# Optimization experiments

Hardware: AMD Instinct MI355X
Metric: run time of the kernel (lower is better)

The kernel has to match this reference:

```python
import jax, jax.numpy as jnp
import numpy as np

H = 4096          # hidden_size
NH = 32           # num_attention_heads
NKV = 2           # multi_query_group_num (kv heads)
HD = 128          # kv_channels / head_dim
RD = 64           # rotary_dim = head_dim * rotary_percent(0.5)
T = 2048          # total tokens (single prefill sequence)
EPS = 1e-5        # layernorm_epsilon
ROPE_BASE = 10000.0


def setup_inputs() -> dict:
    key = jax.random.key(0)
    k0, k1, k2, k3 = jax.random.split(key, 4)
    qkv_out = (NH + 2 * NKV) * HD  # 4608
    return {
        "positions": jnp.arange(T, dtype=jnp.int32),
        "hidden_states": jax.random.normal(k0, (T, H), jnp.float32),
        "w_qkv": jax.random.normal(k1, (qkv_out, H), jnp.float32) * 0.02,
        "b_qkv": jax.random.normal(k2, (qkv_out,), jnp.float32) * 0.02,
        "w_dense": jax.random.normal(k3, (H, NH * HD), jnp.float32) * 0.02,
        "q_ln_w": jnp.ones((HD,), jnp.float32),
        "k_ln_w": jnp.ones((HD,), jnp.float32),
    }


def _rmsnorm(x, w):
    # per-head RMSNorm over head_dim
    return x * jax.lax.rsqrt(jnp.mean(x * x, axis=-1, keepdims=True) + EPS) * w


def _rope(x, positions):
    # partial rotary (first RD dims), interleaved GPT-J style (is_neox_style=False)
    inv_freq = 1.0 / (ROPE_BASE ** (jnp.arange(0, RD, 2, dtype=jnp.float32) / RD))
    ang = positions.astype(jnp.float32)[:, None] * inv_freq      # [T, RD//2]
    cos = jnp.cos(ang)[:, None, :]                               # [T, 1, RD//2]
    sin = jnp.sin(ang)[:, None, :]
    x_rot, x_pass = x[..., :RD], x[..., RD:]
    x1 = x_rot[..., 0::2]
    x2 = x_rot[..., 1::2]
    r1 = x1 * cos - x2 * sin
    r2 = x2 * cos + x1 * sin
    x_rot = jnp.stack([r1, r2], axis=-1).reshape(x.shape[:-1] + (RD,))
    return jnp.concatenate([x_rot, x_pass], axis=-1)


def reference(positions, hidden_states, w_qkv, b_qkv, w_dense, q_ln_w, k_ln_w):
    qkv = hidden_states @ w_qkv.T + b_qkv                        # [T, 4608]
    q_size, kv_size = NH * HD, NKV * HD
    q = qkv[:, :q_size].reshape(T, NH, HD)
    k = qkv[:, q_size:q_size + kv_size].reshape(T, NKV, HD)
    v = qkv[:, q_size + kv_size:].reshape(T, NKV, HD)
    # optional qk layernorm (RMSNorm since config.rmsnorm)
    q = _rmsnorm(q, q_ln_w)
    k = _rmsnorm(k, k_ln_w)
    # rotary embedding
    q = _rope(q, positions)
    k = _rope(k, positions)
    # GQA: expand kv heads to query heads
    group = NH // NKV
    k_exp = jnp.repeat(k, group, axis=1)                         # [T, NH, HD]
    v_exp = jnp.repeat(v, group, axis=1)
    scale = HD ** -0.5
    scores = jnp.einsum("thd,shd->hts", q, k_exp) * scale        # [NH, T, T]
    causal = jnp.tril(jnp.ones((T, T), dtype=bool))
    scores = jnp.where(causal[None, :, :], scores, jnp.finfo(scores.dtype).min)
    attn = jax.nn.softmax(scores, axis=-1)
    out = jnp.einsum("hts,shd->thd", attn, v_exp).reshape(T, NH * HD)
    return out @ w_dense.T                                       # [T, H]
```

## Files before the change

kernel.cpp:

```cpp
#include <hip/hip_runtime.h>
#include <cstdint>
#include <cstddef>

typedef short short4v __attribute__((ext_vector_type(4)));
typedef short short8v __attribute__((ext_vector_type(8)));
typedef float f32x4   __attribute__((ext_vector_type(4)));

#define T_LEN  2048
#define HDIM   4096
#define NHEADS 32
#define HEADD  128
#define QKVN   4608

static __device__ __forceinline__ short f2bf(float f) {
  __bf16 h = (__bf16)f;
  return __builtin_bit_cast(short, h);
}

static __device__ __forceinline__ void gload_lds16(const void* g, void* l) {
  __builtin_amdgcn_global_load_lds((const __attribute__((address_space(1))) void*)g,
                                   (__attribute__((address_space(3))) void*)l,
                                   16, 0, 0);
}

__global__ void cast_f32_to_bf16(const float* __restrict__ in, short* __restrict__ out, int n4) {
  int idx = blockIdx.x * blockDim.x + threadIdx.x;
  int stride = gridDim.x * blockDim.x;
  const float4* in4 = (const float4*)in;
  short4v* out4 = (short4v*)out;
  for (int i = idx; i < n4; i += stride) {
    float4 v = in4[i];
    short4v o;
    o[0] = f2bf(v.x); o[1] = f2bf(v.y); o[2] = f2bf(v.z); o[3] = f2bf(v.w);
    out4[i] = o;
  }
}

__global__ __launch_bounds__(256, 2) void gemm_bt(
    const short* __restrict__ A,
    const short* __restrict__ B,
    const float* __restrict__ bias,
    float* __restrict__ Cout,
    int M, int N, int K)
{
  __shared__ short sA[2][128 * 64];
  __shared__ short sB[2][128 * 64];
  const int tid  = threadIdx.x;
  const int lane = tid & 63;
  const int wv   = tid >> 6;
  const int wr   = wv >> 1;
  const int wc   = wv & 1;
  const int bn0  = blockIdx.x * 128;
  const int bm0  = blockIdx.y * 128;

  const int fr  = lane & 15;
  const int fkb = (lane >> 4) << 4;
  const int swz = (fr & 7) << 4;

  const int c_row  = tid >> 3;
  const int c_colb = (tid & 7) << 4;
  const int c_scol = (c_colb ^ ((c_row & 7) << 4)) >> 1;

  f32x4 zero = {0.f, 0.f, 0.f, 0.f};
  f32x4 acc[4][4];
#pragma unroll
  for (int m = 0; m < 4; m++)
#pragma unroll
    for (int n = 0; n < 4; n++) acc[m][n] = zero;

  auto STAGE = [&](int b, int kt) {
#pragma unroll
    for (int i = 0; i < 4; i++) {
      const int row = i * 32 + c_row;
      gload_lds16(A + (size_t)(bm0 + row) * K + kt + c_scol,
                  (char*)&sA[b][0] + (size_t)(i * 256 + wv * 64) * 16);
    }
#pragma unroll
    for (int i = 0; i < 4; i++) {
      const int row = i * 32 + c_row;
      gload_lds16(B + (size_t)(bn0 + row) * K + kt + c_scol,
                  (char*)&sB[b][0] + (size_t)(i * 256 + wv * 64) * 16);
    }
  };

  int cur = 0;
  STAGE(0, 0);
  __syncthreads();

  for (int kt = 0; kt < K; kt += 64) {
    if (kt + 64 < K) STAGE(cur ^ 1, kt + 64);
    const char* aB = (const char*)&sA[cur][0];
    const char* bB = (const char*)&sB[cur][0];
#pragma unroll
    for (int ks = 0; ks < 2; ks++) {
      short8v af[4], bfr[4];
#pragma unroll
      for (int m = 0; m < 4; m++) {
        const int row = wr * 64 + m * 16 + fr;
        af[m] = *(const short8v*)(aB + row * 128 + ((ks * 64 + fkb) ^ swz));
      }
#pragma unroll
      for (int n = 0; n < 4; n++) {
        const int row = wc * 64 + n * 16 + fr;
        bfr[n] = *(const short8v*)(bB + row * 128 + ((ks * 64 + fkb) ^ swz));
      }
#pragma unroll
      for (int m = 0; m < 4; m++)
#pragma unroll
        for (int n = 0; n < 4; n++)
          acc[m][n] = __builtin_amdgcn_mfma_f32_16x16x32_bf16(af[m], bfr[n], acc[m][n], 0, 0, 0);
    }
    __syncthreads();
    cur ^= 1;
  }

  const int rg = (lane >> 4) * 4;
#pragma unroll
  for (int m = 0; m < 4; m++) {
#pragma unroll
    for (int n = 0; n < 4; n++) {
      const int gcol = bn0 + wc * 64 + n * 16 + fr;
      const float bv = bias ? bias[gcol] : 0.0f;
#pragma unroll
      for (int j = 0; j < 4; j++) {
        const int grow = bm0 + wr * 64 + m * 16 + rg + j;
        Cout[(size_t)grow * N + gcol] = acc[m][n][j] + bv;
      }
    }
  }
}

__global__ __launch_bounds__(64) void qkv_post_kernel(
    const float* __restrict__ qkvf,
    const int*   __restrict__ positions,
    const float* __restrict__ q_ln,
    const float* __restrict__ k_ln,
    short* __restrict__ Qb,
    short* __restrict__ Kb,
    short* __restrict__ Vt)
{
  const int t = blockIdx.x;
  const int h = blockIdx.y;
  const int lane = threadIdx.x;
  const float2 x2 = ((const float2*)(qkvf + (size_t)t * QKVN + h * HEADD))[lane];
  float x = x2.x, y = x2.y;

  if (h >= 34) {
    const int hv = h - 34;
    short* dst = Vt + ((size_t)hv * HEADD + 2 * lane) * T_LEN + t;
    dst[0]     = f2bf(x);
    dst[T_LEN] = f2bf(y);
    return;
  }

  float ss = x * x + y * y;
#pragma unroll
  for (int d = 32; d > 0; d >>= 1) ss += __shfl_xor(ss, d);
  const float r = rsqrtf(ss * (1.0f / 128.0f) + 1e-5f);
  const float* lnw = (h < 32) ? q_ln : k_ln;
  x = x * r * lnw[2 * lane];
  y = y * r * lnw[2 * lane + 1];

  if (lane < 32) {
    const float pos = (float)positions[t];
    const float ang = pos * powf(10000.0f, -(float)lane * (1.0f / 32.0f));
    const float c = cosf(ang), s = sinf(ang);
    const float r1 = x * c - y * s;
    const float r2 = y * c + x * s;
    x = r1; y = r2;
  }

  short* dst = (h < 32) ? (Qb + ((size_t)h * T_LEN + t) * HEADD + 2 * lane)
                        : (Kb + ((size_t)(h - 32) * T_LEN + t) * HEADD + 2 * lane);
  dst[0] = f2bf(x);
  dst[1] = f2bf(y);
}

__global__ __launch_bounds__(256, 2) void attn_kernel(
    const short* __restrict__ Qb,
    const short* __restrict__ Kb,
    const short* __restrict__ Vt,
    short* __restrict__ attn_out)
{
  __shared__ short Ks[2][64 * 128];
  __shared__ short Vs[2][128 * 64];
  __shared__ short pbuf[4][32 * 64];
  const int blk  = gridDim.x - 1 - blockIdx.x;
  const int h    = blockIdx.y;
  const int hkv  = h >> 4;
  const int tid  = threadIdx.x;
  const int lane = tid & 63;
  const int wv   = tid >> 6;
  const int B0   = blk * 128;
  const int qrow0 = B0 + wv * 32;
  const int fr = lane & 15;
  const int fk = (lane >> 4) * 8;
  const int fkb = (lane >> 4) << 4;
  const int rg = (lane >> 4) * 4;
  const int swz = (fr & 7) << 4;

  const short* Kh = Kb + (size_t)hkv * T_LEN * HEADD;
  const short* Vh = Vt + (size_t)hkv * HEADD * T_LEN;

  short8v qf[2][4];
#pragma unroll
  for (int g = 0; g < 2; g++) {
    const short* Qrow = Qb + ((size_t)h * T_LEN + qrow0 + g * 16 + fr) * HEADD + fk;
#pragma unroll
    for (int d0 = 0; d0 < 4; d0++) qf[g][d0] = *(const short8v*)(Qrow + d0 * 32);
  }

  float mrow[2][4], lrow[2][4];
#pragma unroll
  for (int g = 0; g < 2; g++)
#pragma unroll
    for (int j = 0; j < 4; j++) { mrow[g][j] = -1e30f; lrow[g][j] = 0.f; }
  f32x4 zero = {0.f, 0.f, 0.f, 0.f};
  f32x4 o[2][8];
#pragma unroll
  for (int g = 0; g < 2; g++)
#pragma unroll
    for (int d = 0; d < 8; d++) o[g][d] = zero;

  char* pb = (char*)&pbuf[wv][0];
  const float scale = 0.08838834764831845f;
  const int nt = 2 * blk + 2;

  auto STAGE = [&](int b, int t) {
    const int s0 = t * 64;
#pragma unroll
    for (int i = 0; i < 4; i++) {
      const int c    = i * 256 + tid;
      const int row  = c >> 4;
      const int colb = (c & 15) << 4;
      const int scol = (colb ^ ((row & 7) << 4)) >> 1;
      gload_lds16(Kh + (size_t)(s0 + row) * HEADD + scol,
                  (char*)&Ks[b][0] + (size_t)(i * 256 + wv * 64) * 16);
    }
#pragma unroll
    for (int i = 0; i < 4; i++) {
      const int c    = i * 256 + tid;
      const int row  = c >> 3;
      const int colb = (c & 7) << 4;
      const int scol = (colb ^ ((row & 7) << 4)) >> 1;
      gload_lds16(Vh + (size_t)row * T_LEN + s0 + scol,
                  (char*)&Vs[b][0] + (size_t)(i * 256 + wv * 64) * 16);
    }
  };

  int cur = 0;
  STAGE(0, 0);
  __syncthreads();

  for (int t = 0; t < nt; ++t) {
    if (t + 1 < nt) STAGE(cur ^ 1, t + 1);
    const int s0 = t * 64;
    const char* KsB = (const char*)&Ks[cur][0];
    const char* VsB = (const char*)&Vs[cur][0];

    float scv[2][4][4];
#pragma unroll
    for (int sub = 0; sub < 4; sub++) {
      const char* Kbase = KsB + (sub * 16 + fr) * 256;
      f32x4 a0 = zero, a1 = zero;
#pragma unroll
      for (int d0 = 0; d0 < 4; d0++) {
        short8v kf = *(const short8v*)(Kbase + ((d0 * 64 + fkb) ^ swz));
        a0 = __builtin_amdgcn_mfma_f32_16x16x32_bf16(qf[0][d0], kf, a0, 0, 0, 0);
        a1 = __builtin_amdgcn_mfma_f32_16x16x32_bf16(qf[1][d0], kf, a1, 0, 0, 0);
      }
#pragma unroll
      for (int j = 0; j < 4; j++) {
        scv[0][sub][j] = a0[j] * scale;
        scv[1][sub][j] = a1[j] * scale;
      }
    }
    if (t >= nt - 2) {
#pragma unroll
      for (int g = 0; g < 2; g++)
#pragma unroll
        for (int sub = 0; sub < 4; sub++) {
          const int colp = s0 + sub * 16 + fr;
#pragma unroll
          for (int j = 0; j < 4; j++)
            if (colp > qrow0 + g * 16 + rg + j) scv[g][sub][j] = -1e30f;
        }
    }
    float pmax[2][4];
#pragma unroll
    for (int g = 0; g < 2; g++)
#pragma unroll
      for (int j = 0; j < 4; j++)
        pmax[g][j] = fmaxf(fmaxf(scv[g][0][j], scv[g][1][j]),
                           fmaxf(scv[g][2][j], scv[g][3][j]));
    float growth = -1e30f;
#pragma unroll
    for (int g = 0; g < 2; g++)
#pragma unroll
      for (int j = 0; j < 4; j++) growth = fmaxf(growth, pmax[g][j] - mrow[g][j]);
    if (!__all(growth <= 8.0f)) {
#pragma unroll
      for (int g = 0; g < 2; g++)
#pragma unroll
        for (int j = 0; j < 4; j++) {
          float mx = pmax[g][j];
#pragma unroll
          for (int d = 1; d < 16; d <<= 1) mx = fmaxf(mx, __shfl_xor(mx, d));
          const float mn = fmaxf(mrow[g][j], mx);
          const float c  = __expf(mrow[g][j] - mn);
          mrow[g][j] = mn;
          lrow[g][j] *= c;
#pragma unroll
          for (int df = 0; df < 8; df++) o[g][df][j] *= c;
        }
    }
#pragma unroll
    for (int g = 0; g < 2; g++)
#pragma unroll
      for (int j = 0; j < 4; j++) {
        const int prow = g * 16 + rg + j;
        char* prb = pb + prow * 128;
        const int rswz = ((rg + j) & 7) << 4;
        float ps = 0.f;
#pragma unroll
        for (int sub = 0; sub < 4; sub++) {
          const float p = __expf(scv[g][sub][j] - mrow[g][j]);
          ps += p;
          *(short*)(prb + ((((sub * 16 + fr) << 1)) ^ rswz)) = f2bf(p);
        }
        lrow[g][j] += ps;
      }
    asm volatile("" ::: "memory");
    short8v pf[2][2];
#pragma unroll
    for (int g = 0; g < 2; g++)
#pragma unroll
      for (int ks = 0; ks < 2; ks++)
        pf[g][ks] = *(const short8v*)(pb + (g * 16 + fr) * 128 + ((ks * 64 + fkb) ^ swz));
#pragma unroll
    for (int df = 0; df < 8; df++) {
      const char* Vbase = VsB + (df * 16 + fr) * 128;
      short8v vf0 = *(const short8v*)(Vbase + ((0 + fkb) ^ swz));
      short8v vf1 = *(const short8v*)(Vbase + ((64 + fkb) ^ swz));
      o[0][df] = __builtin_amdgcn_mfma_f32_16x16x32_bf16(pf[0][0], vf0, o[0][df], 0, 0, 0);
      o[0][df] = __builtin_amdgcn_mfma_f32_16x16x32_bf16(pf[0][1], vf1, o[0][df], 0, 0, 0);
      o[1][df] = __builtin_amdgcn_mfma_f32_16x16x32_bf16(pf[1][0], vf0, o[1][df], 0, 0, 0);
      o[1][df] = __builtin_amdgcn_mfma_f32_16x16x32_bf16(pf[1][1], vf1, o[1][df], 0, 0, 0);
    }
    __syncthreads();
    cur ^= 1;
  }

#pragma unroll
  for (int g = 0; g < 2; g++)
#pragma unroll
    for (int j = 0; j < 4; j++) {
#pragma unroll
      for (int d = 1; d < 16; d <<= 1) lrow[g][j] += __shfl_xor(lrow[g][j], d);
    }
#pragma unroll
  for (int g = 0; g < 2; g++)
#pragma unroll
    for (int df = 0; df < 8; df++)
#pragma unroll
      for (int j = 0; j < 4; j++) {
        const float v = o[g][df][j] / lrow[g][j];
        attn_out[(size_t)(qrow0 + g * 16 + rg + j) * HDIM + h * HEADD + df * 16 + fr] = f2bf(v);
      }
}

extern "C" void kernel_launch(void* const* d_in, const int* in_sizes, int n_in,
                              void* d_out, int out_size, void* d_ws, size_t ws_size,
                              hipStream_t stream) {
  (void)out_size; (void)ws_size;
  int ip = 0, ih = 1, iwq = 2, ib = 3, iwd = 4, il0 = 5, il1 = 6;
  if (n_in == 7) {
    int p = -1, hh = -1, wq = -1, b = -1, wd = -1, l0 = -1, l1 = -1, ok = 1;
    for (int i = 0; i < 7; i++) {
      switch (in_sizes[i]) {
        case 2048:     p  = i; break;
        case 8388608:  hh = i; break;
        case 18874368: wq = i; break;
        case 4608:     b  = i; break;
        case 16777216: wd = i; break;
        case 128:      if (l0 < 0) l0 = i; else l1 = i; break;
        default:       ok = 0; break;
      }
    }
    if (ok && p >= 0 && hh >= 0 && wq >= 0 && b >= 0 && wd >= 0 && l0 >= 0 && l1 >= 0) {
      ip = p; ih = hh; iwq = wq; ib = b; iwd = wd; il0 = l0; il1 = l1;
    }
  }

  const int*   positions = (const int*)d_in[ip];
  const float* hidden    = (const float*)d_in[ih];
  const float* w_qkv     = (const float*)d_in[iwq];
  const float* b_qkv     = (const float*)d_in[ib];
  const float* w_dense   = (const float*)d_in[iwd];
  const float* q_ln      = (const float*)d_in[il0];
  const float* k_ln      = (const float*)d_in[il1];

  char* ws = (char*)d_ws;
  short* Ahs   = (short*)(ws + 0);
  short* Qb    = (short*)(ws + 0);
  short* Wqkv  = (short*)(ws + (size_t)16777216);
  short* Kb    = (short*)(ws + (size_t)16777216);
  short* Vt    = (short*)(ws + (size_t)17825792);
  short* Wd    = (short*)(ws + (size_t)18874368);
  float* qkvf  = (float*)(ws + (size_t)54525952);
  short* attnb = (short*)(ws + (size_t)54525952);

  cast_f32_to_bf16<<<dim3(1024), dim3(256), 0, stream>>>(hidden, Ahs, (T_LEN * HDIM) / 4);
  cast_f32_to_bf16<<<dim3(2048), dim3(256), 0, stream>>>(w_qkv, Wqkv, (QKVN * HDIM) / 4);
  gemm_bt<<<dim3(QKVN / 128, T_LEN / 128), dim3(256), 0, stream>>>(
      Ahs, Wqkv, b_qkv, qkvf, T_LEN, QKVN, HDIM);
  qkv_post_kernel<<<dim3(T_LEN, 36), dim3(64), 0, stream>>>(
      qkvf, positions, q_ln, k_ln, Qb, Kb, Vt);
  cast_f32_to_bf16<<<dim3(2048), dim3(256), 0, stream>>>(w_dense, Wd, (HDIM * HDIM) / 4);
  attn_kernel<<<dim3(16, NHEADS), dim3(256), 0, stream>>>(Qb, Kb, Vt, attnb);
  gemm_bt<<<dim3(HDIM / 128, T_LEN / 128), dim3(256), 0, stream>>>(
      attnb, Wd, nullptr, (float*)d_out, T_LEN, HDIM, HDIM);
}
```

Baseline: 366.2 us.

## Emit bf16 QKV output, remap GEMM workgroups, single-buffer LDS staging

The QKV projection GEMM now writes bf16 instead of fp32, and the post-processing kernel reads packed bf16 pairs. This halves the traffic of that intermediate tensor but rounds q/k/v before RMSNorm. The GEMM also remaps workgroup IDs in groups of eight to change tile scheduling order, aiming at better L2 reuse. It drops double-buffered LDS for a single buffer with a sync after each stage. That halves LDS use, which may allow more occupancy, but loads no longer overlap with MFMA compute.

```diff
diff --git a/kernel.cpp b/kernel.cpp
--- a/kernel.cpp
+++ b/kernel.cpp
@@ -15,6 +15,9 @@
 static __device__ __forceinline__ short f2bf(float f) {
   __bf16 h = (__bf16)f;
   return __builtin_bit_cast(short, h);
+}
+static __device__ __forceinline__ float bf2f(short u) {
+  return __builtin_bit_cast(float, ((unsigned int)(unsigned short)u) << 16);
 }
 
 static __device__ __forceinline__ void gload_lds16(const void* g, void* l) {
@@ -36,22 +39,27 @@
   }
 }
 
+template <int OUT_BF16>
 __global__ __launch_bounds__(256, 2) void gemm_bt(
     const short* __restrict__ A,
     const short* __restrict__ B,
     const float* __restrict__ bias,
-    float* __restrict__ Cout,
+    void* __restrict__ Cout,
     int M, int N, int K)
 {
-  __shared__ short sA[2][128 * 64];
-  __shared__ short sB[2][128 * 64];
+  __shared__ short sA[128 * 64];
+  __shared__ short sB[128 * 64];
   const int tid  = threadIdx.x;
   const int lane = tid & 63;
   const int wv   = tid >> 6;
   const int wr   = wv >> 1;
   const int wc   = wv & 1;
-  const int bn0  = blockIdx.x * 128;
-  const int bm0  = blockIdx.y * 128;
+
+  const int nwg  = gridDim.x * gridDim.y;
+  int wgid = blockIdx.y * gridDim.x + blockIdx.x;
+  wgid = (wgid & 7) * (nwg >> 3) + (wgid >> 3);
+  const int bn0 = (wgid / gridDim.y) * 128;
+  const int bm0 = (wgid % gridDim.y) * 128;
 
   const int fr  = lane & 15;
   const int fkb = (lane >> 4) << 4;
@@ -61,36 +69,29 @@
   const int c_colb = (tid & 7) << 4;
   const int c_scol = (c_colb ^ ((c_row & 7) << 4)) >> 1;
 
-  f32x4 zero = {0.f, 0.f, 0.f, 0.f};
-  f32x4 acc[4][4];
-#pragma unroll
-  for (int m = 0; m < 4; m++)
-#pragma unroll
-    for (int n = 0; n < 4; n++) acc[m][n] = zero;
-
-  auto STAGE = [&](int b, int kt) {
+  auto STAGE = [&](int kt) {
 #pragma unroll
     for (int i = 0; i < 4; i++) {
       const int row = i * 32 + c_row;
       gload_lds16(A + (size_t)(bm0 + row) * K + kt + c_scol,
-                  (char*)&sA[b][0] + (size_t)(i * 256 + wv * 64) * 16);
-    }
-#pragma unroll
-    for (int i = 0; i < 4; i++) {
-      const int row = i * 32 + c_row;
+                  (char*)sA + (size_t)(i * 256 + wv * 64) * 16);
       gload_lds16(B + (size_t)(bn0 + row) * K + kt + c_scol,
-                  (char*)&sB[b][0] + (size_t)(i * 256 + wv * 64) * 16);
+                  (char*)sB + (size_t)(i * 256 + wv * 64) * 16);
     }
   };
 
-  int cur = 0;
-  STAGE(0, 0);
-  __syncthreads();
+  f32x4 zero = {0.f, 0.f, 0.f, 0.f};
+  f32x4 acc[4][4];
+#pragma unroll
+  for (int m = 0; m < 4; m++)
+#pragma unroll
+    for (int n = 0; n < 4; n++) acc[m][n] = zero;
 
   for (int kt = 0; kt < K; kt += 64) {
-    if (kt + 64 < K) STAGE(cur ^ 1, kt + 64);
-    const char* aB = (const char*)&sA[cur][0];
-    const char* bB = (const char*)&sB[cur][0];
+    STAGE(kt);
+    __syncthreads();
+    const char* aB = (const char*)sA;
+    const char* bB = (const char*)sB;
 #pragma unroll
     for (int ks = 0; ks < 2; ks++) {
       short8v af[4], bfr[4];
@@ -111,7 +112,6 @@
           acc[m][n] = __builtin_amdgcn_mfma_f32_16x16x32_bf16(af[m], bfr[n], acc[m][n], 0, 0, 0);
     }
     __syncthreads();
-    cur ^= 1;
   }
 
   const int rg = (lane >> 4) * 4;
@@ -124,14 +124,18 @@
 #pragma unroll
       for (int j = 0; j < 4; j++) {
         const int grow = bm0 + wr * 64 + m * 16 + rg + j;
-        Cout[(size_t)grow * N + gcol] = acc[m][n][j] + bv;
+        const float v = acc[m][n][j] + bv;
+        if (OUT_BF16)
+          ((short*)Cout)[(size_t)grow * N + gcol] = f2bf(v);
+        else
+          ((float*)Cout)[(size_t)grow * N + gcol] = v;
       }
     }
   }
 }
 
 __global__ __launch_bounds__(64) void qkv_post_kernel(
-    const float* __restrict__ qkvf,
+    const short* __restrict__ qkvb,
     const int*   __restrict__ positions,
     const float* __restrict__ q_ln,
     const float* __restrict__ k_ln,
@@ -142,8 +146,10 @@
   const int t = blockIdx.x;
   const int h = blockIdx.y;
   const int lane = threadIdx.x;
-  const float2 x2 = ((const float2*)(qkvf + (size_t)t * QKVN + h * HEADD))[lane];
-  float x = x2.x, y = x2.y;
+  const unsigned int pk =
+      ((const unsigned int*)(qkvb + (size_t)t * QKVN + h * HEADD))[lane];
+  float x = bf2f((short)(pk & 0xffffu));
+  float y = bf2f((short)(pk >> 16));
 
   if (h >= 34) {
     const int hv = h - 34;
@@ -407,17 +413,17 @@
   short* Kb    = (short*)(ws + (size_t)16777216);
   short* Vt    = (short*)(ws + (size_t)17825792);
   short* Wd    = (short*)(ws + (size_t)18874368);
-  float* qkvf  = (float*)(ws + (size_t)54525952);
+  short* qkvb  = (short*)(ws + (size_t)54525952);
   short* attnb = (short*)(ws + (size_t)54525952);
 
   cast_f32_to_bf16<<<dim3(1024), dim3(256), 0, stream>>>(hidden, Ahs, (T_LEN * HDIM) / 4);
   cast_f32_to_bf16<<<dim3(2048), dim3(256), 0, stream>>>(w_qkv, Wqkv, (QKVN * HDIM) / 4);
-  gemm_bt<<<dim3(QKVN / 128, T_LEN / 128), dim3(256), 0, stream>>>(
-      Ahs, Wqkv, b_qkv, qkvf, T_LEN, QKVN, HDIM);
+  gemm_bt<1><<<dim3(QKVN / 128, T_LEN / 128), dim3(256), 0, stream>>>(
+      Ahs, Wqkv, b_qkv, (void*)qkvb, T_LEN, QKVN, HDIM);
   qkv_post_kernel<<<dim3(T_LEN, 36), dim3(64), 0, stream>>>(
-      qkvf, positions, q_ln, k_ln, Qb, Kb, Vt);
+      qkvb, positions, q_ln, k_ln, Qb, Kb, Vt);
   cast_f32_to_bf16<<<dim3(2048), dim3(256), 0, stream>>>(w_dense, Wd, (HDIM * HDIM) / 4);
   attn_kernel<<<dim3(16, NHEADS), dim3(256), 0, stream>>>(Qb, Kb, Vt, attnb);
-  gemm_bt<<<dim3(HDIM / 128, T_LEN / 128), dim3(256), 0, stream>>>(
-      attnb, Wd, nullptr, (float*)d_out, T_LEN, HDIM, HDIM);
-}
+  gemm_bt<0><<<dim3(HDIM / 128, T_LEN / 128), dim3(256), 0, stream>>>(
+      attnb, Wd, nullptr, d_out, T_LEN, HDIM, HDIM);
+}
```

Result: faster. 324.7 us (-11.3%).
